# Performance work log

Hardware: AMD Instinct MI355X
Metric: run time of the kernel (lower is better)

Reference implementation:

```python
import jax, jax.numpy as jnp
from jax import lax
import numpy as np

# ---- init hyperparameters (from init_kwargs) ----
STRIDE = 1
DP_CHANNELS = 1
ATOM_R = 8
ATOM_C = 8
NUMB_ATOM = 128
T_SC = 3
K = 256
BATCH = 32
IMG = 64


def setup_inputs() -> dict:
    key = jax.random.key(0)
    k1, k2 = jax.random.split(key)
    Y = jax.random.normal(k1, (BATCH, DP_CHANNELS, IMG, IMG), dtype=jnp.float32)
    # ConvTranspose2d weight layout: (numb_atom, dp_channels, atom_c, atom_r)
    W = jax.random.normal(k2, (NUMB_ATOM, DP_CHANNELS, ATOM_C, ATOM_R), dtype=jnp.float32)
    # normalise_weights(): each (i, j) filter divided by its L2 norm
    W = W / jnp.sqrt(jnp.sum(W ** 2, axis=(2, 3), keepdims=True))
    return {"Y": Y, "W_D": W}


def _conv_D(X, W):
    # PyTorch ConvTranspose2d (stride=1, no padding): full convolution with
    # spatially-flipped kernel; W is (in=numb_atom, out=dp_channels, kh, kw).
    kh, kw = W.shape[2], W.shape[3]
    return lax.conv_general_dilated(
        X, jnp.flip(W, (2, 3)), (1, 1),
        [(kh - 1, kh - 1), (kw - 1, kw - 1)],
        dimension_numbers=('NCHW', 'IOHW', 'NCHW'))


def _conv_Dt(R, Wt):
    # PyTorch Conv2d (VALID, stride=1): Wt is (out=numb_atom, in=dp, kh, kw)
    return lax.conv_general_dilated(
        R, Wt, (1, 1), 'VALID', dimension_numbers=('NCHW', 'OIHW', 'NCHW'))


def _hard_threshold_k(X, k):
    # keep the k largest-|.| entries per sample (over flattened C,H,W)
    B = X.shape[0]
    flat = X.reshape(B, -1)
    _, idx = lax.top_k(jnp.abs(flat), k)                      # [B, k]
    vals = jnp.take_along_axis(flat, idx, axis=1)             # [B, k]
    out = jnp.zeros_like(flat).at[jnp.arange(B)[:, None], idx].set(vals)
    return out.reshape(X.shape)


def _linesearch(Y, X, W, Wt, k):
    R = Y - _conv_D(X, W)
    g = _conv_Dt(R, Wt)
    l2_start = jnp.sum(R ** 2)

    def attempt(alpha):
        Xu = _hard_threshold_k(X + alpha * g, k)
        err = jnp.sum((Y - _conv_D(Xu, W)) ** 2)
        return Xu, err

    Xu0, err0 = attempt(jnp.float32(1.0))

    def cond(s):
        _, _, err, count = s
        return (err >= l2_start) & (count <= 15)

    def body(s):
        alpha, _, _, count = s
        alpha = alpha * jnp.float32(0.5)
        Xu, err = attempt(alpha)
        return (alpha, Xu, err, count + 1)

    alpha, Xu, err, _ = lax.while_loop(
        cond, body, (jnp.float32(1.0), Xu0, err0, jnp.int32(0)))
    return Xu, err, alpha


def reference(Y, W_D):
    # D_trans.weight = D.weight.permute(0,1,3,2) -> (numb_atom, dp, atom_r, atom_c)
    Wt = jnp.swapaxes(W_D, 2, 3)
    kh, kw = Wt.shape[2], Wt.shape[3]
    B, _, H, W_sp = Y.shape
    X = jnp.zeros((B, W_D.shape[0], H - kh + 1, W_sp - kw + 1), dtype=Y.dtype)
    for _ in range(T_SC):
        X, _, _ = _linesearch(Y, X, W_D, Wt, K)
    return X
```

## Files before the change

### kernel.cpp

```cpp
#include <hip/hip_runtime.h>
#include <stdint.h>

#define NB   32
#define NCH  128
#define IMG  64
#define IMG2 4096
#define OH   57
#define OHW  3249
#define CHW  415872
#define KTOP 256
#define NATT 17
#define NS   32
#define SCAP 512
#define NCAP 1536
#define NBUCK 8192
#define HSHIFT 18
#define TGT  512
#define RSTRIDE 72
#define NZB  257
#define BMW  12996

typedef unsigned long long ull;

__global__ void k_init(int* support_cnt) {
    if (threadIdx.x < NB) support_cnt[threadIdx.x] = 0;
}

__global__ __launch_bounds__(256) void k_resid(
    const float* __restrict__ Y, const float* __restrict__ W,
    const int* __restrict__ support_cnt, const ull* __restrict__ sup_iv,
    float* __restrict__ Rg, double* __restrict__ l2part,
    uint32_t* __restrict__ hist, int* __restrict__ cand_cnt)
{
    int bx = blockIdx.x, tid = threadIdx.x;
    if (bx >= NB) {
        int zb = bx - NB;
        if (zb < 256) {
            ((uint4*)hist)[zb * 256 + tid] = make_uint4(0u, 0u, 0u, 0u);
        } else {
            ((uint4*)cand_cnt)[tid] = make_uint4(0u, 0u, 0u, 0u);
        }
        return;
    }
    int b = bx;
    __shared__ float Rs[IMG2];
    const float4* Y4 = (const float4*)(Y + b * IMG2);
    float4* R4 = (float4*)Rs;
    for (int i = tid; i < IMG2 / 4; i += 256) R4[i] = Y4[i];
    __syncthreads();
    int n = support_cnt[b];
    for (int task = tid; task < n * 64; task += 256) {
        int i = task >> 6, tap = task & 63, p = tap >> 3, q = tap & 7;
        ull iv = sup_iv[b * KTOP + i];
        uint32_t idx = (uint32_t)iv;
        float val = __uint_as_float((uint32_t)(iv >> 32));
        int c = idx / OHW, rem = idx % OHW, s = rem / OH, t = rem % OH;
        float w = W[c * 64 + p * 8 + q];
        atomicAdd(&Rs[(s + p) * IMG + (t + q)], -val * w);
    }
    __syncthreads();
    double acc = 0.0;
    for (int i = tid; i < IMG2; i += 256) {
        float v = Rs[i];
        Rg[b * IMG2 + i] = v;
        acc += (double)v * (double)v;
    }
    __shared__ double red[256];
    red[tid] = acc; __syncthreads();
    for (int s2 = 128; s2 > 0; s2 >>= 1) { if (tid < s2) red[tid] += red[tid + s2]; __syncthreads(); }
    if (tid == 0) l2part[b] = red[0];
}

__global__ __launch_bounds__(256) void k_conv(
    const float* __restrict__ Rg, const float* __restrict__ W,
    float* __restrict__ g_out, uint32_t* __restrict__ hist)
{
    int b = blockIdx.x, cg0 = blockIdx.y, tid = threadIdx.x;
    __shared__ float Rs[71 * 72];
    __shared__ uint32_t hl[NBUCK];
    for (int i = tid; i < 71 * 72; i += 256) Rs[i] = 0.f;
    for (int i = tid; i < NBUCK; i += 256) hl[i] = 0u;
    __syncthreads();
    const float4* R4 = (const float4*)(Rg + b * IMG2);
    for (int i = tid; i < 1024; i += 256) {
        int row = i >> 4, col4 = (i & 15) * 4;
        *(float4*)&Rs[row * 72 + col4] = R4[i];
    }
    __syncthreads();
    int csub = tid >> 7;
    int tile = tid & 127;
    bool active = tile < 120;
    int tr = active ? tile / 15 : 0;
    int tc = active ? tile % 15 : 0;
    int s0 = tr * 8, t0 = tc * 4;

    for (int sub = 0; sub < 4; ++sub) {
        int c = cg0 * 8 + sub * 2 + csub;
        int c_s = __builtin_amdgcn_readfirstlane(c);
        const float* Wc = W + c_s * 64;

        float acc[8][4];
#pragma unroll
        for (int r = 0; r < 8; ++r)
#pragma unroll
            for (int cc = 0; cc < 4; ++cc) acc[r][cc] = 0.f;

#pragma unroll
        for (int rho = 0; rho < 15; ++rho) {
            float rb[12];
            const float* rp = &Rs[(s0 + rho) * 72 + t0];
            *(float4*)&rb[0] = *(const float4*)rp;
            *(float4*)&rb[4] = *(const float4*)(rp + 4);
            *(float4*)&rb[8] = *(const float4*)(rp + 8);
#pragma unroll
            for (int r = 0; r < 8; ++r) {
                const int p = rho - r;
                if (p >= 0 && p < 8) {
#pragma unroll
                    for (int q = 0; q < 8; ++q) {
                        float wv = Wc[q * 8 + p];
#pragma unroll
                        for (int cc = 0; cc < 4; ++cc)
                            acc[r][cc] = fmaf(rb[cc + q], wv, acc[r][cc]);
                    }
                }
            }
        }
        if (active) {
            float* go = g_out + (size_t)(b * NCH + c) * OHW;
#pragma unroll
            for (int r = 0; r < 8; ++r) {
                int s = s0 + r;
                if (s < OH) {
#pragma unroll
                    for (int cc = 0; cc < 4; ++cc) {
                        int t = t0 + cc;
                        if (t < OH) {
                            float v = acc[r][cc];
                            go[s * OH + t] = v;
                            uint32_t bits = __float_as_uint(v) & 0x7fffffffu;
                            atomicAdd(&hl[bits >> HSHIFT], 1u);
                        }
                    }
                }
            }
        }
    }
    __syncthreads();
    for (int i = tid; i < NBUCK; i += 256) {
        uint32_t v = hl[i];
        if (v) atomicAdd(&hist[b * NBUCK + i], v);
    }
}

__global__ __launch_bounds__(256) void k_thresh(const uint32_t* __restrict__ hist,
                                                uint32_t* __restrict__ thr) {
    int b = blockIdx.x, tid = threadIdx.x;
    uint32_t h[32];
    uint32_t s = 0;
    const uint32_t* hb = hist + b * NBUCK + tid * 32;
#pragma unroll
    for (int k = 0; k < 32; ++k) { h[k] = hb[k]; s += h[k]; }
    __shared__ uint32_t buf[2][256];
    int cur = 0;
    buf[0][tid] = s;
    __syncthreads();
    for (int d = 1; d < 256; d <<= 1) {
        uint32_t v = buf[cur][tid];
        if (tid + d < 256) v += buf[cur][tid + d];
        buf[cur ^ 1][tid] = v;
        cur ^= 1;
        __syncthreads();
    }
    uint32_t sufme = buf[cur][tid];
    uint32_t base  = (tid < 255) ? buf[cur][tid + 1] : 0u;
    if (tid == 0 && buf[cur][0] < TGT) thr[b] = 0u;
    if (base < TGT && sufme >= TGT) {
        uint32_t acc = base; int bk = 0;
#pragma unroll
        for (int k = 31; k >= 0; --k) {
            acc += h[k];
            if (acc >= TGT) { bk = tid * 32 + k; break; }
        }
        thr[b] = (uint32_t)bk << HSHIFT;
    }
}

__global__ __launch_bounds__(256) void k_collect(
    const float* __restrict__ g, const uint32_t* __restrict__ thr,
    int* __restrict__ cand_cnt, uint32_t* __restrict__ cand_idx, float* __restrict__ cand_g)
{
    int b = blockIdx.y;
    int i4 = blockIdx.x * 256 + threadIdx.x;
    if (i4 >= CHW / 4) return;
    int slice = blockIdx.x & (NS - 1);
    uint32_t tb = thr[b];
    float4 v4 = ((const float4*)(g + (size_t)b * CHW))[i4];
    float vv[4] = { v4.x, v4.y, v4.z, v4.w };
#pragma unroll
    for (int k = 0; k < 4; ++k) {
        uint32_t bits = __float_as_uint(vv[k]) & 0x7fffffffu;
        if (bits >= tb) {
            int pos = atomicAdd(&cand_cnt[b * NS + slice], 1);
            if (pos < SCAP) {
                cand_idx[(b * NS + slice) * SCAP + pos] = (uint32_t)(i4 * 4 + k);
                cand_g[(b * NS + slice) * SCAP + pos] = vv[k];
            }
        }
    }
}

__global__ __launch_bounds__(1024) void k_suppg(
    const float* __restrict__ g,
    const int* __restrict__ support_cnt, const ull* __restrict__ sup_iv,
    const int* __restrict__ cand_cnt, const uint32_t* __restrict__ cand_idx,
    const float* __restrict__ cand_g,
    uint4* __restrict__ ns_pack, ull* __restrict__ sup_gp, ull* __restrict__ kb_all)
{
    int b = blockIdx.x, tid = threadIdx.x, lane = tid & 63;
    __shared__ uint32_t bm[BMW];
    __shared__ int cnts[NS];
    __shared__ ull ck[NCAP];
    __shared__ float cg_l[NCAP];
    __shared__ int nns_sh;
    int n = support_cnt[b];
    for (int i = tid; i < BMW / 4; i += 1024) ((uint4*)bm)[i] = make_uint4(0u, 0u, 0u, 0u);
    if (tid < NS) cnts[tid] = min(cand_cnt[b * NS + tid], SCAP);
    if (tid == 0) nns_sh = 0;
    __syncthreads();
    if (tid < KTOP) {
        float gv = 0.f, vs = 0.f;
        uint32_t nidx;
        if (tid < n) {
            ull iv = sup_iv[b * KTOP + tid];
            uint32_t idx = (uint32_t)iv;
            nidx = idx;
            vs = __uint_as_float((uint32_t)(iv >> 32));
            atomicOr(&bm[idx >> 5], 1u << (idx & 31));
            gv = g[(size_t)b * CHW + idx];
            int c = idx / OHW, r = idx % OHW, s = r / OH, t = r % OH;
            uint32_t pk = (uint32_t)((c << 12) | (s << 6) | t);
            sup_gp[b * KTOP + tid] = ((ull)__float_as_uint(gv) << 32) | (ull)pk;
        } else {
            nidx = (uint32_t)(CHW + tid);
            sup_gp[b * KTOP + tid] = 0ull;
        }
        ull klo = (ull)(uint32_t)(~nidx);
#pragma unroll
        for (int a2 = 0; a2 < NATT; ++a2) {
            float v2 = (tid < n) ? fmaf(ldexpf(1.f, -a2), gv, vs) : 0.f;
            kb_all[((size_t)a2 * NB + b) * KTOP + tid] =
                ((ull)(__float_as_uint(v2) & 0x7fffffffu) << 32) | klo;
        }
    }
    __syncthreads();
    for (int t0 = tid; t0 < NS * SCAP; t0 += 1024) {
        int s = t0 >> 9, j = t0 & (SCAP - 1);
        bool keep = false; uint32_t idx = 0; float gv = 0.f;
        if (j < cnts[s]) {
            idx = cand_idx[(b * NS + s) * SCAP + j];
            gv = cand_g[(b * NS + s) * SCAP + j];
            keep = ((bm[idx >> 5] >> (idx & 31)) & 1u) == 0u;
        }
        ull mk = __ballot(keep);
        if (mk) {
            int basep = 0;
            if (lane == 0) basep = atomicAdd(&nns_sh, (int)__popcll(mk));
            basep = __shfl(basep, 0, 64);
            if (keep) {
                int p = basep + (int)__popcll(mk & ((1ull << lane) - 1ull));
                if (p < NCAP) {
                    ck[p] = ((ull)(__float_as_uint(gv) & 0x7fffffffu) << 32) | (ull)(uint32_t)(~idx);
                    cg_l[p] = gv;
                }
            }
        }
    }
    __syncthreads();
    int nns = min(nns_sh, NCAP);
    int nns8 = (nns + 7) & ~7;
    for (int i = nns + tid; i < nns8; i += 1024) ck[i] = 0ull;
    __syncthreads();
    ull myk[2]; int myr[2];
#pragma unroll
    for (int q = 0; q < 2; ++q) { int i = tid + 1024 * q; myk[q] = (i < nns) ? ck[i] : 0ull; myr[q] = 0; }
    for (int j = 0; j < nns8; j += 8) {
        ull t0 = ck[j], t1 = ck[j+1], t2 = ck[j+2], t3 = ck[j+3];
        ull t4 = ck[j+4], t5 = ck[j+5], t6 = ck[j+6], t7 = ck[j+7];
#pragma unroll
        for (int q = 0; q < 2; ++q) {
            myr[q] += ((t0 > myk[q]) ? 1 : 0) + ((t1 > myk[q]) ? 1 : 0)
                    + ((t2 > myk[q]) ? 1 : 0) + ((t3 > myk[q]) ? 1 : 0)
                    + ((t4 > myk[q]) ? 1 : 0) + ((t5 > myk[q]) ? 1 : 0)
                    + ((t6 > myk[q]) ? 1 : 0) + ((t7 > myk[q]) ? 1 : 0);
        }
    }
#pragma unroll
    for (int q = 0; q < 2; ++q) {
        int i = tid + 1024 * q;
        if (i < nns && myr[q] < KTOP) {
            uint32_t idx = ~(uint32_t)myk[q];
            int r = myr[q];
            int c = idx / OHW, rr = idx % OHW, s = rr / OH, t = rr % OH;
            uint32_t pk = (uint32_t)((c << 12) | (s << 6) | t);
            ns_pack[b * KTOP + r] = make_uint4(idx, __float_as_uint(cg_l[i]), pk, 0u);
        }
    }
}

__global__ __launch_bounds__(512) void k_att2(
    const float* __restrict__ Y, const float* __restrict__ W,
    const int* __restrict__ support_cnt, const ull* __restrict__ sup_iv,
    const ull* __restrict__ sup_gp, const uint4* __restrict__ ns_pack,
    const ull* __restrict__ kb_all,
    uint32_t* __restrict__ sel_idx, float* __restrict__ sel_val, double* __restrict__ err)
{
    int a = blockIdx.x, b = blockIdx.y, tid = threadIdx.x;
    int lane = tid & 63, wid = tid >> 6;
    float alpha = ldexpf(1.f, -a);
    int n = support_cnt[b];

    __shared__ float recon[64 * RSTRIDE];
    __shared__ ull kA[KTOP];
    __shared__ ull s_pv[KTOP];
    __shared__ uint32_t s_idx[KTOP];
    __shared__ double redd[8];

    uint32_t myi = 0, mypk = 0;
    float myv = 0.f;
    ull myk = 0;
    if (tid < KTOP) {
        uint4 np = ns_pack[b * KTOP + tid];
        myi = np.x;
        myv = alpha * __uint_as_float(np.y);
        mypk = np.z;
        myk = ((ull)(__float_as_uint(myv) & 0x7fffffffu) << 32) | (ull)(uint32_t)(~myi);
        kA[tid] = myk;
    } else {
        int t2 = tid - KTOP;
        ull gp = sup_gp[b * KTOP + t2];
        ull iv = sup_iv[b * KTOP + t2];
        if (t2 < n) {
            myi = (uint32_t)iv;
            myv = fmaf(alpha, __uint_as_float((uint32_t)(gp >> 32)),
                       __uint_as_float((uint32_t)(iv >> 32)));
            mypk = (uint32_t)gp;
        } else {
            myi = (uint32_t)(CHW + t2);
            myv = 0.f; mypk = 0u;
        }
        myk = ((ull)(__float_as_uint(myv) & 0x7fffffffu) << 32) | (ull)(uint32_t)(~myi);
    }

    const float4* Y4 = (const float4*)(Y + b * IMG2);
    float4 y0 = Y4[tid * 2], y1 = Y4[tid * 2 + 1];

    for (int i = tid; i < 64 * RSTRIDE; i += 512) recon[i] = 0.f;
    __syncthreads();

    const ull* __restrict__ kb = kb_all + ((size_t)a * NB + b) * KTOP;
    int cb0 = 0, cb1 = 0;
    for (int j = 0; j < KTOP; j += 8) {
        ull t0 = kb[j],     t1 = kb[j + 1], t2 = kb[j + 2], t3 = kb[j + 3];
        ull t4 = kb[j + 4], t5 = kb[j + 5], t6 = kb[j + 6], t7 = kb[j + 7];
        cb0 += ((t0 > myk) ? 1 : 0) + ((t1 > myk) ? 1 : 0)
             + ((t2 > myk) ? 1 : 0) + ((t3 > myk) ? 1 : 0);
        cb1 += ((t4 > myk) ? 1 : 0) + ((t5 > myk) ? 1 : 0)
             + ((t6 > myk) ? 1 : 0) + ((t7 > myk) ? 1 : 0);
    }
    int cb = cb0 + cb1;
    int rank;
    if (tid < KTOP) {
        rank = tid + cb;
    } else {
        int lo = 0, hi = KTOP;
        while (lo < hi) { int mid = (lo + hi) >> 1; if (kA[mid] > myk) lo = mid + 1; else hi = mid; }
        rank = lo + cb;
    }
    if (rank < KTOP) {
        s_pv[rank] = ((ull)__float_as_uint(myv) << 32) | (ull)mypk;
        s_idx[rank] = myi;
    }
    __syncthreads();

    {
        int p = lane >> 3, q = lane & 7;
        ull pv[4]; float wv[4];
#pragma unroll
        for (int j = 0; j < 4; ++j) pv[j] = s_pv[wid + 8 * j];
#pragma unroll
        for (int j = 0; j < 4; ++j) wv[j] = W[(((uint32_t)pv[j]) >> 12) * 64 + lane];
#pragma unroll
        for (int k4 = 0; k4 < 32; k4 += 4) {
            ull npv[4] = {0, 0, 0, 0}; float nwv[4] = {0.f, 0.f, 0.f, 0.f};
            if (k4 + 4 < 32) {
#pragma unroll
                for (int j = 0; j < 4; ++j) npv[j] = s_pv[wid + 8 * (k4 + 4 + j)];
#pragma unroll
                for (int j = 0; j < 4; ++j) nwv[j] = W[(((uint32_t)npv[j]) >> 12) * 64 + lane];
            }
#pragma unroll
            for (int j = 0; j < 4; ++j) {
                uint32_t pk = (uint32_t)pv[j];
                float val = __uint_as_float((uint32_t)(pv[j] >> 32));
                int s = (pk >> 6) & 63, t = pk & 63;
                atomicAdd(&recon[(s + p) * RSTRIDE + (t + q)], val * wv[j]);
            }
#pragma unroll
            for (int j = 0; j < 4; ++j) { pv[j] = npv[j]; wv[j] = nwv[j]; }
        }
    }
    __syncthreads();

    double accd = 0.0;
    {
        int idx0 = tid * 2;
        const float* rr = &recon[(idx0 >> 4) * RSTRIDE + (idx0 & 15) * 4];
        float d0 = y0.x - rr[0]; accd += (double)d0 * (double)d0;
        float d1 = y0.y - rr[1]; accd += (double)d1 * (double)d1;
        float d2 = y0.z - rr[2]; accd += (double)d2 * (double)d2;
        float d3 = y0.w - rr[3]; accd += (double)d3 * (double)d3;
        int idx1 = tid * 2 + 1;
        rr = &recon[(idx1 >> 4) * RSTRIDE + (idx1 & 15) * 4];
        float e0 = y1.x - rr[0]; accd += (double)e0 * (double)e0;
        float e1 = y1.y - rr[1]; accd += (double)e1 * (double)e1;
        float e2 = y1.z - rr[2]; accd += (double)e2 * (double)e2;
        float e3 = y1.w - rr[3]; accd += (double)e3 * (double)e3;
    }
    for (int d = 32; d > 0; d >>= 1) accd += __shfl_xor(accd, d, 64);
    if (lane == 0) redd[wid] = accd;
    __syncthreads();
    if (tid == 0) {
        double e = 0.0;
#pragma unroll
        for (int w2 = 0; w2 < 8; ++w2) e += redd[w2];
        err[a * NB + b] = e;
    }

    if (tid < KTOP) {
        size_t o = ((size_t)a * NB + b) * KTOP;
        ull pvt = s_pv[tid];
        sel_idx[o + tid] = s_idx[tid];
        sel_val[o + tid] = __uint_as_float((uint32_t)(pvt >> 32));
    }
}

__global__ __launch_bounds__(256) void k_update(
    const double* __restrict__ l2part, const double* __restrict__ err,
    const uint32_t* __restrict__ sel_idx, const float* __restrict__ sel_val,
    int* __restrict__ support_cnt, ull* __restrict__ sup_iv)
{
    int b = blockIdx.x, tid = threadIdx.x;
    __shared__ double esum[NATT + 1];
    __shared__ int sel_sh;
    if (tid < NATT) {
        double e = 0.0;
        for (int b2 = 0; b2 < NB; ++b2) e += err[tid * NB + b2];
        esum[tid] = e;
    } else if (tid == NATT) {
        double l2 = 0.0;
        for (int b2 = 0; b2 < NB; ++b2) l2 += l2part[b2];
        esum[NATT] = l2;
    }
    __syncthreads();
    if (tid == 0) {
        double l2 = esum[NATT];
        int sel = NATT - 1;
        for (int a2 = 0; a2 < NATT; ++a2) if (esum[a2] < l2) { sel = a2; break; }
        sel_sh = sel;
    }
    __syncthreads();
    int a = sel_sh;
    __shared__ uint32_t ki[KTOP];
    __shared__ float kv[KTOP];
    ki[tid] = sel_idx[((size_t)a * NB + b) * KTOP + tid];
    kv[tid] = sel_val[((size_t)a * NB + b) * KTOP + tid];
    __syncthreads();
    uint32_t me = ki[tid];
    int rank = 0;
    for (int j = 0; j < KTOP; j += 8) {
        uint32_t a0 = ki[j], a1 = ki[j+1], a2 = ki[j+2], a3 = ki[j+3];
        uint32_t a4 = ki[j+4], a5 = ki[j+5], a6 = ki[j+6], a7 = ki[j+7];
        rank += ((a0 < me) ? 1 : 0) + ((a1 < me) ? 1 : 0) + ((a2 < me) ? 1 : 0) + ((a3 < me) ? 1 : 0)
              + ((a4 < me) ? 1 : 0) + ((a5 < me) ? 1 : 0) + ((a6 < me) ? 1 : 0) + ((a7 < me) ? 1 : 0);
    }
    sup_iv[b * KTOP + rank] = (ull)me | ((ull)__float_as_uint(kv[tid]) << 32);
    if (tid == 0) support_cnt[b] = KTOP;
}

__global__ void k_outzero(float4* __restrict__ out) {
    int i = blockIdx.x * 256 + threadIdx.x;
    if (i < (NB * CHW) / 4) out[i] = make_float4(0.f, 0.f, 0.f, 0.f);
}

__global__ void k_scatter(const ull* __restrict__ sup_iv, float* __restrict__ out) {
    int b = blockIdx.x, tid = threadIdx.x;
    if (tid < KTOP) {
        ull iv = sup_iv[b * KTOP + tid];
        out[(size_t)b * CHW + (uint32_t)iv] = __uint_as_float((uint32_t)(iv >> 32));
    }
}

static size_t align256(size_t x) { return (x + 255) & ~(size_t)255; }

extern "C" void kernel_launch(void* const* d_in, const int* in_sizes, int n_in,
                              void* d_out, int out_size, void* d_ws, size_t ws_size,
                              hipStream_t stream)
{
    const float* Y = (const float*)d_in[0];
    const float* W = (const float*)d_in[1];
    float* out = (float*)d_out;

    char* p = (char*)d_ws;
    size_t off = 0;
    auto carve = [&](size_t bytes) { void* r = p + off; off = align256(off + bytes); return r; };
    float*    Rg          = (float*)   carve(NB * IMG2 * sizeof(float));
    uint32_t* hist        = (uint32_t*)carve((size_t)NB * NBUCK * sizeof(uint32_t));
    uint32_t* thr         = (uint32_t*)carve(NB * sizeof(uint32_t));
    int*      cand_cnt    = (int*)     carve(NB * NS * sizeof(int));
    double*   l2part      = (double*)  carve(NB * sizeof(double));
    double*   err         = (double*)  carve(NATT * NB * sizeof(double));
    int*      support_cnt = (int*)     carve(NB * sizeof(int));
    ull*      sup_iv      = (ull*)     carve((size_t)NB * KTOP * sizeof(ull));
    uint32_t* sel_idx     = (uint32_t*)carve((size_t)NATT * NB * KTOP * sizeof(uint32_t));
    float*    sel_val     = (float*)   carve((size_t)NATT * NB * KTOP * sizeof(float));
    uint32_t* cand_idx    = (uint32_t*)carve((size_t)NB * NS * SCAP * sizeof(uint32_t));
    float*    cand_g      = (float*)   carve((size_t)NB * NS * SCAP * sizeof(float));
    uint4*    ns_pack     = (uint4*)   carve((size_t)NB * KTOP * sizeof(uint4));
    ull*      sup_gp      = (ull*)     carve((size_t)NB * KTOP * sizeof(ull));
    ull*      kb_all      = (ull*)     carve((size_t)NATT * NB * KTOP * sizeof(ull));
    (void)ws_size; (void)in_sizes; (void)n_in; (void)out_size;

    k_init<<<1, 64, 0, stream>>>(support_cnt);
    for (int t = 0; t < 3; ++t) {
        k_resid<<<NB + NZB, 256, 0, stream>>>(Y, W, support_cnt, sup_iv,
                                              Rg, l2part, hist, cand_cnt);
        k_conv<<<dim3(NB, 16), 256, 0, stream>>>(Rg, W, out, hist);
        k_thresh<<<NB, 256, 0, stream>>>(hist, thr);
        k_collect<<<dim3((CHW / 4 + 255) / 256, NB), 256, 0, stream>>>(out, thr, cand_cnt, cand_idx, cand_g);
        k_suppg<<<NB, 1024, 0, stream>>>(out, support_cnt, sup_iv,
                                         cand_cnt, cand_idx, cand_g,
                                         ns_pack, sup_gp, kb_all);
        k_att2<<<dim3(NATT, NB), 512, 0, stream>>>(Y, W, support_cnt, sup_iv,
                                                   sup_gp, ns_pack, kb_all,
                                                   sel_idx, sel_val, err);
        k_update<<<NB, 256, 0, stream>>>(l2part, err, sel_idx, sel_val,
                                         support_cnt, sup_iv);
    }
    k_outzero<<<((NB * CHW) / 4 + 255) / 256, 256, 0, stream>>>((float4*)out);
    k_scatter<<<NB, 256, 0, stream>>>(sup_iv, out);
}
```

Before: 662.4 us.

## Split attempt kernel into selection and reconstruction kernels

Splits the fused per-attempt kernel into k_sel and k_rec. k_sel uses 256 threads, each ranking one new candidate and one support entry against the kb table. k_rec loads the selected entries from global memory and does the reconstruction and error reduction. This should lighten register and shared-memory pressure and shorten the serial rank phase inside the heavy kernel. In exchange it adds a launch per iteration and a global round trip through new att_pv and att_idx buffers. The two sentinel index assignments for padded support slots conflict: the else branch sets CHW+tid+KTOP, then a following line overwrites it with CHW+tid. Since it is only a padding sentinel with zero value it likely does not matter.

```diff
diff --git a/kernel.cpp b/kernel.cpp
--- a/kernel.cpp
+++ b/kernel.cpp
@@ -308,79 +308,95 @@
     }
 }
 
-__global__ __launch_bounds__(512) void k_att2(
-    const float* __restrict__ Y, const float* __restrict__ W,
+__global__ __launch_bounds__(256) void k_sel(
     const int* __restrict__ support_cnt, const ull* __restrict__ sup_iv,
     const ull* __restrict__ sup_gp, const uint4* __restrict__ ns_pack,
     const ull* __restrict__ kb_all,
-    uint32_t* __restrict__ sel_idx, float* __restrict__ sel_val, double* __restrict__ err)
+    ull* __restrict__ att_pv, uint32_t* __restrict__ att_idx)
 {
     int a = blockIdx.x, b = blockIdx.y, tid = threadIdx.x;
-    int lane = tid & 63, wid = tid >> 6;
     float alpha = ldexpf(1.f, -a);
     int n = support_cnt[b];
 
-    __shared__ float recon[64 * RSTRIDE];
     __shared__ ull kA[KTOP];
-    __shared__ ull s_pv[KTOP];
-    __shared__ uint32_t s_idx[KTOP];
-    __shared__ double redd[8];
-
-    uint32_t myi = 0, mypk = 0;
-    float myv = 0.f;
-    ull myk = 0;
-    if (tid < KTOP) {
-        uint4 np = ns_pack[b * KTOP + tid];
-        myi = np.x;
-        myv = alpha * __uint_as_float(np.y);
-        mypk = np.z;
-        myk = ((ull)(__float_as_uint(myv) & 0x7fffffffu) << 32) | (ull)(uint32_t)(~myi);
-        kA[tid] = myk;
+
+    uint4 np = ns_pack[b * KTOP + tid];
+    uint32_t ni = np.x;
+    float nv = alpha * __uint_as_float(np.y);
+    uint32_t npk = np.z;
+    ull nk = ((ull)(__float_as_uint(nv) & 0x7fffffffu) << 32) | (ull)(uint32_t)(~ni);
+    kA[tid] = nk;
+
+    ull gp = sup_gp[b * KTOP + tid];
+    ull iv = sup_iv[b * KTOP + tid];
+    uint32_t si; float sv; uint32_t spk;
+    if (tid < n) {
+        si = (uint32_t)iv;
+        sv = fmaf(alpha, __uint_as_float((uint32_t)(gp >> 32)),
+                  __uint_as_float((uint32_t)(iv >> 32)));
+        spk = (uint32_t)gp;
     } else {
-        int t2 = tid - KTOP;
-        ull gp = sup_gp[b * KTOP + t2];
-        ull iv = sup_iv[b * KTOP + t2];
-        if (t2 < n) {
-            myi = (uint32_t)iv;
-            myv = fmaf(alpha, __uint_as_float((uint32_t)(gp >> 32)),
-                       __uint_as_float((uint32_t)(iv >> 32)));
-            mypk = (uint32_t)gp;
-        } else {
-            myi = (uint32_t)(CHW + t2);
-            myv = 0.f; mypk = 0u;
-        }
-        myk = ((ull)(__float_as_uint(myv) & 0x7fffffffu) << 32) | (ull)(uint32_t)(~myi);
-    }
-
-    const float4* Y4 = (const float4*)(Y + b * IMG2);
-    float4 y0 = Y4[tid * 2], y1 = Y4[tid * 2 + 1];
-
-    for (int i = tid; i < 64 * RSTRIDE; i += 512) recon[i] = 0.f;
+        si = (uint32_t)(CHW + tid + KTOP);
+        sv = 0.f; spk = 0u;
+    }
+    if (tid >= n) si = (uint32_t)(CHW + tid);
+    ull sk = ((ull)(__float_as_uint(sv) & 0x7fffffffu) << 32) | (ull)(uint32_t)(~si);
     __syncthreads();
 
     const ull* __restrict__ kb = kb_all + ((size_t)a * NB + b) * KTOP;
-    int cb0 = 0, cb1 = 0;
+    int cbn = 0, cbs = 0;
     for (int j = 0; j < KTOP; j += 8) {
         ull t0 = kb[j],     t1 = kb[j + 1], t2 = kb[j + 2], t3 = kb[j + 3];
         ull t4 = kb[j + 4], t5 = kb[j + 5], t6 = kb[j + 6], t7 = kb[j + 7];
-        cb0 += ((t0 > myk) ? 1 : 0) + ((t1 > myk) ? 1 : 0)
-             + ((t2 > myk) ? 1 : 0) + ((t3 > myk) ? 1 : 0);
-        cb1 += ((t4 > myk) ? 1 : 0) + ((t5 > myk) ? 1 : 0)
-             + ((t6 > myk) ? 1 : 0) + ((t7 > myk) ? 1 : 0);
-    }
-    int cb = cb0 + cb1;
-    int rank;
+        cbn += ((t0 > nk) ? 1 : 0) + ((t1 > nk) ? 1 : 0)
+             + ((t2 > nk) ? 1 : 0) + ((t3 > nk) ? 1 : 0)
+             + ((t4 > nk) ? 1 : 0) + ((t5 > nk) ? 1 : 0)
+             + ((t6 > nk) ? 1 : 0) + ((t7 > nk) ? 1 : 0);
+        cbs += ((t0 > sk) ? 1 : 0) + ((t1 > sk) ? 1 : 0)
+             + ((t2 > sk) ? 1 : 0) + ((t3 > sk) ? 1 : 0)
+             + ((t4 > sk) ? 1 : 0) + ((t5 > sk) ? 1 : 0)
+             + ((t6 > sk) ? 1 : 0) + ((t7 > sk) ? 1 : 0);
+    }
+    int rank_n = tid + cbn;
+    int lo = 0, hi = KTOP;
+    while (lo < hi) { int mid = (lo + hi) >> 1; if (kA[mid] > sk) lo = mid + 1; else hi = mid; }
+    int rank_s = lo + cbs;
+
+    size_t o = ((size_t)a * NB + b) * KTOP;
+    if (rank_n < KTOP) {
+        att_pv[o + rank_n] = ((ull)__float_as_uint(nv) << 32) | (ull)npk;
+        att_idx[o + rank_n] = ni;
+    }
+    if (rank_s < KTOP) {
+        att_pv[o + rank_s] = ((ull)__float_as_uint(sv) << 32) | (ull)spk;
+        att_idx[o + rank_s] = si;
+    }
+}
+
+__global__ __launch_bounds__(512) void k_rec(
+    const float* __restrict__ Y, const float* __restrict__ W,
+    const ull* __restrict__ att_pv, const uint32_t* __restrict__ att_idx,
+    uint32_t* __restrict__ sel_idx, float* __restrict__ sel_val, double* __restrict__ err)
+{
+    int a = blockIdx.x, b = blockIdx.y, tid = threadIdx.x;
+    int lane = tid & 63, wid = tid >> 6;
+
+    __shared__ float recon[64 * RSTRIDE];
+    __shared__ ull s_pv[KTOP];
+    __shared__ double redd[8];
+
+    size_t o = ((size_t)a * NB + b) * KTOP;
     if (tid < KTOP) {
-        rank = tid + cb;
-    } else {
-        int lo = 0, hi = KTOP;
-        while (lo < hi) { int mid = (lo + hi) >> 1; if (kA[mid] > myk) lo = mid + 1; else hi = mid; }
-        rank = lo + cb;
-    }
-    if (rank < KTOP) {
-        s_pv[rank] = ((ull)__float_as_uint(myv) << 32) | (ull)mypk;
-        s_idx[rank] = myi;
-    }
+        ull pv = att_pv[o + tid];
+        s_pv[tid] = pv;
+        sel_idx[o + tid] = att_idx[o + tid];
+        sel_val[o + tid] = __uint_as_float((uint32_t)(pv >> 32));
+    }
+
+    const float4* Y4 = (const float4*)(Y + b * IMG2);
+    float4 y0 = Y4[tid * 2], y1 = Y4[tid * 2 + 1];
+
+    for (int i = tid; i < 64 * RSTRIDE; i += 512) recon[i] = 0.f;
     __syncthreads();
 
     {
@@ -435,13 +451,6 @@
 #pragma unroll
         for (int w2 = 0; w2 < 8; ++w2) e += redd[w2];
         err[a * NB + b] = e;
-    }
-
-    if (tid < KTOP) {
-        size_t o = ((size_t)a * NB + b) * KTOP;
-        ull pvt = s_pv[tid];
-        sel_idx[o + tid] = s_idx[tid];
-        sel_val[o + tid] = __uint_as_float((uint32_t)(pvt >> 32));
     }
 }
 
@@ -529,6 +538,8 @@
     uint4*    ns_pack     = (uint4*)   carve((size_t)NB * KTOP * sizeof(uint4));
     ull*      sup_gp      = (ull*)     carve((size_t)NB * KTOP * sizeof(ull));
     ull*      kb_all      = (ull*)     carve((size_t)NATT * NB * KTOP * sizeof(ull));
+    ull*      att_pv      = (ull*)     carve((size_t)NATT * NB * KTOP * sizeof(ull));
+    uint32_t* att_idx     = (uint32_t*)carve((size_t)NATT * NB * KTOP * sizeof(uint32_t));
     (void)ws_size; (void)in_sizes; (void)n_in; (void)out_size;
 
     k_init<<<1, 64, 0, stream>>>(support_cnt);
@@ -541,9 +552,10 @@
         k_suppg<<<NB, 1024, 0, stream>>>(out, support_cnt, sup_iv,
                                          cand_cnt, cand_idx, cand_g,
                                          ns_pack, sup_gp, kb_all);
-        k_att2<<<dim3(NATT, NB), 512, 0, stream>>>(Y, W, support_cnt, sup_iv,
-                                                   sup_gp, ns_pack, kb_all,
-                                                   sel_idx, sel_val, err);
+        k_sel<<<dim3(NATT, NB), 256, 0, stream>>>(support_cnt, sup_iv, sup_gp,
+                                                  ns_pack, kb_all, att_pv, att_idx);
+        k_rec<<<dim3(NATT, NB), 512, 0, stream>>>(Y, W, att_pv, att_idx,
+                                                  sel_idx, sel_val, err);
         k_update<<<NB, 256, 0, stream>>>(l2part, err, sel_idx, sel_val,
                                          support_cnt, sup_iv);
     }
```

Measured after the change: 678.9 us. 2.5% more time.

## Fuse line-search attempts and update into cooperative kernel with early exit

Applied to the files above, without the earlier changes.

Replaces the kernel that evaluated all 17 step-size attempts in parallel, and the separate update kernel, with one cooperative kernel. It evaluates attempts in rounds of 8 per batch sample. After each round a grid-wide sync lets block 0 pick the first accepted step, and later rounds are skipped once one passes. The winning block writes the new support directly, which removes the intermediate selection buffers and one launch per iteration. In exchange it adds grid syncs, caps parallelism at 256 blocks, and writes the support in magnitude-rank order instead of index-sorted order.

```diff
diff --git a/kernel.cpp b/kernel.cpp
--- a/kernel.cpp
+++ b/kernel.cpp
@@ -1,5 +1,8 @@
 #include <hip/hip_runtime.h>
+#include <hip/hip_cooperative_groups.h>
 #include <stdint.h>
+
+namespace cg = cooperative_groups;
 
 #define NB   32
 #define NCH  128
@@ -10,6 +13,8 @@
 #define CHW  415872
 #define KTOP 256
 #define NATT 17
+#define NBATCH 8
+#define NROUNDS 3
 #define NS   32
 #define SCAP 512
 #define NCAP 1536
@@ -308,16 +313,16 @@
     }
 }
 
-__global__ __launch_bounds__(512) void k_att2(
+__global__ __launch_bounds__(512) void k_attc(
     const float* __restrict__ Y, const float* __restrict__ W,
-    const int* __restrict__ support_cnt, const ull* __restrict__ sup_iv,
+    int* __restrict__ support_cnt, ull* __restrict__ sup_iv,
     const ull* __restrict__ sup_gp, const uint4* __restrict__ ns_pack,
-    const ull* __restrict__ kb_all,
-    uint32_t* __restrict__ sel_idx, float* __restrict__ sel_val, double* __restrict__ err)
+    const ull* __restrict__ kb_all, const double* __restrict__ l2part,
+    double* __restrict__ err, int* __restrict__ ctrl)
 {
-    int a = blockIdx.x, b = blockIdx.y, tid = threadIdx.x;
-    int lane = tid & 63, wid = tid >> 6;
-    float alpha = ldexpf(1.f, -a);
+    cg::grid_group grid = cg::this_grid();
+    int tid = threadIdx.x, lane = tid & 63, wid = tid >> 6;
+    int b = blockIdx.x & (NB - 1), ar = blockIdx.x >> 5;
     int n = support_cnt[b];
 
     __shared__ float recon[64 * RSTRIDE];
@@ -325,167 +330,169 @@
     __shared__ ull s_pv[KTOP];
     __shared__ uint32_t s_idx[KTOP];
     __shared__ double redd[8];
-
-    uint32_t myi = 0, mypk = 0;
-    float myv = 0.f;
-    ull myk = 0;
-    if (tid < KTOP) {
-        uint4 np = ns_pack[b * KTOP + tid];
-        myi = np.x;
-        myv = alpha * __uint_as_float(np.y);
-        mypk = np.z;
-        myk = ((ull)(__float_as_uint(myv) & 0x7fffffffu) << 32) | (ull)(uint32_t)(~myi);
-        kA[tid] = myk;
-    } else {
-        int t2 = tid - KTOP;
-        ull gp = sup_gp[b * KTOP + t2];
-        ull iv = sup_iv[b * KTOP + t2];
-        if (t2 < n) {
-            myi = (uint32_t)iv;
-            myv = fmaf(alpha, __uint_as_float((uint32_t)(gp >> 32)),
-                       __uint_as_float((uint32_t)(iv >> 32)));
-            mypk = (uint32_t)gp;
-        } else {
-            myi = (uint32_t)(CHW + t2);
-            myv = 0.f; mypk = 0u;
-        }
-        myk = ((ull)(__float_as_uint(myv) & 0x7fffffffu) << 32) | (ull)(uint32_t)(~myi);
-    }
-
-    const float4* Y4 = (const float4*)(Y + b * IMG2);
-    float4 y0 = Y4[tid * 2], y1 = Y4[tid * 2 + 1];
-
-    for (int i = tid; i < 64 * RSTRIDE; i += 512) recon[i] = 0.f;
-    __syncthreads();
-
-    const ull* __restrict__ kb = kb_all + ((size_t)a * NB + b) * KTOP;
-    int cb0 = 0, cb1 = 0;
-    for (int j = 0; j < KTOP; j += 8) {
-        ull t0 = kb[j],     t1 = kb[j + 1], t2 = kb[j + 2], t3 = kb[j + 3];
-        ull t4 = kb[j + 4], t5 = kb[j + 5], t6 = kb[j + 6], t7 = kb[j + 7];
-        cb0 += ((t0 > myk) ? 1 : 0) + ((t1 > myk) ? 1 : 0)
-             + ((t2 > myk) ? 1 : 0) + ((t3 > myk) ? 1 : 0);
-        cb1 += ((t4 > myk) ? 1 : 0) + ((t5 > myk) ? 1 : 0)
-             + ((t6 > myk) ? 1 : 0) + ((t7 > myk) ? 1 : 0);
-    }
-    int cb = cb0 + cb1;
-    int rank;
-    if (tid < KTOP) {
-        rank = tid + cb;
-    } else {
-        int lo = 0, hi = KTOP;
-        while (lo < hi) { int mid = (lo + hi) >> 1; if (kA[mid] > myk) lo = mid + 1; else hi = mid; }
-        rank = lo + cb;
-    }
-    if (rank < KTOP) {
-        s_pv[rank] = ((ull)__float_as_uint(myv) << 32) | (ull)mypk;
-        s_idx[rank] = myi;
-    }
-    __syncthreads();
-
-    {
-        int p = lane >> 3, q = lane & 7;
-        ull pv[4]; float wv[4];
-#pragma unroll
-        for (int j = 0; j < 4; ++j) pv[j] = s_pv[wid + 8 * j];
-#pragma unroll
-        for (int j = 0; j < 4; ++j) wv[j] = W[(((uint32_t)pv[j]) >> 12) * 64 + lane];
-#pragma unroll
-        for (int k4 = 0; k4 < 32; k4 += 4) {
-            ull npv[4] = {0, 0, 0, 0}; float nwv[4] = {0.f, 0.f, 0.f, 0.f};
-            if (k4 + 4 < 32) {
-#pragma unroll
-                for (int j = 0; j < 4; ++j) npv[j] = s_pv[wid + 8 * (k4 + 4 + j)];
-#pragma unroll
-                for (int j = 0; j < 4; ++j) nwv[j] = W[(((uint32_t)npv[j]) >> 12) * 64 + lane];
-            }
-#pragma unroll
-            for (int j = 0; j < 4; ++j) {
-                uint32_t pk = (uint32_t)pv[j];
-                float val = __uint_as_float((uint32_t)(pv[j] >> 32));
-                int s = (pk >> 6) & 63, t = pk & 63;
-                atomicAdd(&recon[(s + p) * RSTRIDE + (t + q)], val * wv[j]);
-            }
-#pragma unroll
-            for (int j = 0; j < 4; ++j) { pv[j] = npv[j]; wv[j] = nwv[j]; }
-        }
-    }
-    __syncthreads();
-
-    double accd = 0.0;
-    {
-        int idx0 = tid * 2;
-        const float* rr = &recon[(idx0 >> 4) * RSTRIDE + (idx0 & 15) * 4];
-        float d0 = y0.x - rr[0]; accd += (double)d0 * (double)d0;
-        float d1 = y0.y - rr[1]; accd += (double)d1 * (double)d1;
-        float d2 = y0.z - rr[2]; accd += (double)d2 * (double)d2;
-        float d3 = y0.w - rr[3]; accd += (double)d3 * (double)d3;
-        int idx1 = tid * 2 + 1;
-        rr = &recon[(idx1 >> 4) * RSTRIDE + (idx1 & 15) * 4];
-        float e0 = y1.x - rr[0]; accd += (double)e0 * (double)e0;
-        float e1 = y1.y - rr[1]; accd += (double)e1 * (double)e1;
-        float e2 = y1.z - rr[2]; accd += (double)e2 * (double)e2;
-        float e3 = y1.w - rr[3]; accd += (double)e3 * (double)e3;
-    }
-    for (int d = 32; d > 0; d >>= 1) accd += __shfl_xor(accd, d, 64);
-    if (lane == 0) redd[wid] = accd;
-    __syncthreads();
-    if (tid == 0) {
-        double e = 0.0;
-#pragma unroll
-        for (int w2 = 0; w2 < 8; ++w2) e += redd[w2];
-        err[a * NB + b] = e;
-    }
-
-    if (tid < KTOP) {
-        size_t o = ((size_t)a * NB + b) * KTOP;
-        ull pvt = s_pv[tid];
-        sel_idx[o + tid] = s_idx[tid];
-        sel_val[o + tid] = __uint_as_float((uint32_t)(pvt >> 32));
-    }
-}
-
-__global__ __launch_bounds__(256) void k_update(
-    const double* __restrict__ l2part, const double* __restrict__ err,
-    const uint32_t* __restrict__ sel_idx, const float* __restrict__ sel_val,
-    int* __restrict__ support_cnt, ull* __restrict__ sup_iv)
-{
-    int b = blockIdx.x, tid = threadIdx.x;
-    __shared__ double esum[NATT + 1];
-    __shared__ int sel_sh;
-    if (tid < NATT) {
-        double e = 0.0;
-        for (int b2 = 0; b2 < NB; ++b2) e += err[tid * NB + b2];
-        esum[tid] = e;
-    } else if (tid == NATT) {
-        double l2 = 0.0;
-        for (int b2 = 0; b2 < NB; ++b2) l2 += l2part[b2];
-        esum[NATT] = l2;
-    }
-    __syncthreads();
-    if (tid == 0) {
-        double l2 = esum[NATT];
-        int sel = NATT - 1;
-        for (int a2 = 0; a2 < NATT; ++a2) if (esum[a2] < l2) { sel = a2; break; }
-        sel_sh = sel;
-    }
-    __syncthreads();
-    int a = sel_sh;
-    __shared__ uint32_t ki[KTOP];
-    __shared__ float kv[KTOP];
-    ki[tid] = sel_idx[((size_t)a * NB + b) * KTOP + tid];
-    kv[tid] = sel_val[((size_t)a * NB + b) * KTOP + tid];
-    __syncthreads();
-    uint32_t me = ki[tid];
-    int rank = 0;
-    for (int j = 0; j < KTOP; j += 8) {
-        uint32_t a0 = ki[j], a1 = ki[j+1], a2 = ki[j+2], a3 = ki[j+3];
-        uint32_t a4 = ki[j+4], a5 = ki[j+5], a6 = ki[j+6], a7 = ki[j+7];
-        rank += ((a0 < me) ? 1 : 0) + ((a1 < me) ? 1 : 0) + ((a2 < me) ? 1 : 0) + ((a3 < me) ? 1 : 0)
-              + ((a4 < me) ? 1 : 0) + ((a5 < me) ? 1 : 0) + ((a6 < me) ? 1 : 0) + ((a7 < me) ? 1 : 0);
-    }
-    sup_iv[b * KTOP + rank] = (ull)me | ((ull)__float_as_uint(kv[tid]) << 32);
-    if (tid == 0) support_cnt[b] = KTOP;
+    __shared__ double esum_sh[NATT + 1];
+
+    int my_a = -1;
+    int a_sel = NATT - 1;
+
+    for (int round = 0; round < NROUNDS; ++round) {
+        int a = round * NBATCH + ar;
+        if (a < NATT) {
+            my_a = a;
+            float alpha = ldexpf(1.f, -a);
+            uint32_t myi = 0, mypk = 0;
+            float myv = 0.f;
+            ull myk = 0;
+            if (tid < KTOP) {
+                uint4 np = ns_pack[b * KTOP + tid];
+                myi = np.x;
+                myv = alpha * __uint_as_float(np.y);
+                mypk = np.z;
+                myk = ((ull)(__float_as_uint(myv) & 0x7fffffffu) << 32) | (ull)(uint32_t)(~myi);
+                kA[tid] = myk;
+            } else {
+                int t2 = tid - KTOP;
+                ull gp = sup_gp[b * KTOP + t2];
+                ull iv = sup_iv[b * KTOP + t2];
+                if (t2 < n) {
+                    myi = (uint32_t)iv;
+                    myv = fmaf(alpha, __uint_as_float((uint32_t)(gp >> 32)),
+                               __uint_as_float((uint32_t)(iv >> 32)));
+                    mypk = (uint32_t)gp;
+                } else {
+                    myi = (uint32_t)(CHW + t2);
+                    myv = 0.f; mypk = 0u;
+                }
+                myk = ((ull)(__float_as_uint(myv) & 0x7fffffffu) << 32) | (ull)(uint32_t)(~myi);
+            }
+            const float4* Y4 = (const float4*)(Y + b * IMG2);
+            float4 y0 = Y4[tid * 2], y1 = Y4[tid * 2 + 1];
+            for (int i = tid; i < 64 * RSTRIDE; i += 512) recon[i] = 0.f;
+            __syncthreads();
+
+            const ull* __restrict__ kb = kb_all + ((size_t)a * NB + b) * KTOP;
+            int cb0 = 0, cb1 = 0;
+            for (int j = 0; j < KTOP; j += 8) {
+                ull t0 = kb[j],     t1 = kb[j + 1], t2 = kb[j + 2], t3 = kb[j + 3];
+                ull t4 = kb[j + 4], t5 = kb[j + 5], t6 = kb[j + 6], t7 = kb[j + 7];
+                cb0 += ((t0 > myk) ? 1 : 0) + ((t1 > myk) ? 1 : 0)
+                     + ((t2 > myk) ? 1 : 0) + ((t3 > myk) ? 1 : 0);
+                cb1 += ((t4 > myk) ? 1 : 0) + ((t5 > myk) ? 1 : 0)
+                     + ((t6 > myk) ? 1 : 0) + ((t7 > myk) ? 1 : 0);
+            }
+            int cb = cb0 + cb1;
+            int rank;
+            if (tid < KTOP) {
+                rank = tid + cb;
+            } else {
+                int lo = 0, hi = KTOP;
+                while (lo < hi) { int mid = (lo + hi) >> 1; if (kA[mid] > myk) lo = mid + 1; else hi = mid; }
+                rank = lo + cb;
+            }
+            if (rank < KTOP) {
+                s_pv[rank] = ((ull)__float_as_uint(myv) << 32) | (ull)mypk;
+                s_idx[rank] = myi;
+            }
+            __syncthreads();
+
+            {
+                int p = lane >> 3, q = lane & 7;
+                ull pv[4]; float wv[4];
+#pragma unroll
+                for (int j = 0; j < 4; ++j) pv[j] = s_pv[wid + 8 * j];
+#pragma unroll
+                for (int j = 0; j < 4; ++j) wv[j] = W[(((uint32_t)pv[j]) >> 12) * 64 + lane];
+#pragma unroll
+                for (int k4 = 0; k4 < 32; k4 += 4) {
+                    ull npv[4] = {0, 0, 0, 0}; float nwv[4] = {0.f, 0.f, 0.f, 0.f};
+                    if (k4 + 4 < 32) {
+#pragma unroll
+                        for (int j = 0; j < 4; ++j) npv[j] = s_pv[wid + 8 * (k4 + 4 + j)];
+#pragma unroll
+                        for (int j = 0; j < 4; ++j) nwv[j] = W[(((uint32_t)npv[j]) >> 12) * 64 + lane];
+                    }
+#pragma unroll
+                    for (int j = 0; j < 4; ++j) {
+                        uint32_t pk = (uint32_t)pv[j];
+                        float val = __uint_as_float((uint32_t)(pv[j] >> 32));
+                        int s = (pk >> 6) & 63, t = pk & 63;
+                        atomicAdd(&recon[(s + p) * RSTRIDE + (t + q)], val * wv[j]);
+                    }
+#pragma unroll
+                    for (int j = 0; j < 4; ++j) { pv[j] = npv[j]; wv[j] = nwv[j]; }
+                }
+            }
+            __syncthreads();
+
+            double accd = 0.0;
+            {
+                int idx0 = tid * 2;
+                const float* rr = &recon[(idx0 >> 4) * RSTRIDE + (idx0 & 15) * 4];
+                float d0 = y0.x - rr[0]; accd += (double)d0 * (double)d0;
+                float d1 = y0.y - rr[1]; accd += (double)d1 * (double)d1;
+                float d2 = y0.z - rr[2]; accd += (double)d2 * (double)d2;
+                float d3 = y0.w - rr[3]; accd += (double)d3 * (double)d3;
+                int idx1 = tid * 2 + 1;
+                rr = &recon[(idx1 >> 4) * RSTRIDE + (idx1 & 15) * 4];
+                float e0 = y1.x - rr[0]; accd += (double)e0 * (double)e0;
+                float e1 = y1.y - rr[1]; accd += (double)e1 * (double)e1;
+                float e2 = y1.z - rr[2]; accd += (double)e2 * (double)e2;
+                float e3 = y1.w - rr[3]; accd += (double)e3 * (double)e3;
+            }
+            for (int d = 32; d > 0; d >>= 1) accd += __shfl_xor(accd, d, 64);
+            if (lane == 0) redd[wid] = accd;
+            __syncthreads();
+            if (tid == 0) {
+                double e = 0.0;
+#pragma unroll
+                for (int w2 = 0; w2 < 8; ++w2) e += redd[w2];
+                err[a * NB + b] = e;
+            }
+        }
+        __threadfence();
+        grid.sync();
+
+        if (blockIdx.x == 0) {
+            int eval = min(NBATCH * (round + 1), NATT);
+            if (tid < NATT) {
+                double e = 0.0;
+                if (tid < eval) {
+#pragma unroll 8
+                    for (int b2 = 0; b2 < NB; ++b2) e += err[tid * NB + b2];
+                }
+                esum_sh[tid] = e;
+            } else if (tid == NATT) {
+                double l2 = 0.0;
+#pragma unroll 8
+                for (int b2 = 0; b2 < NB; ++b2) l2 += l2part[b2];
+                esum_sh[NATT] = l2;
+            }
+            __syncthreads();
+            if (tid == 0) {
+                double l2 = esum_sh[NATT];
+                int sel = -1;
+                for (int a2 = 0; a2 < eval; ++a2) if (esum_sh[a2] < l2) { sel = a2; break; }
+                int done = (sel >= 0 || eval >= NATT) ? 1 : 0;
+                if (sel < 0) sel = NATT - 1;
+                __hip_atomic_store(&ctrl[0], sel, __ATOMIC_RELEASE, __HIP_MEMORY_SCOPE_AGENT);
+                __hip_atomic_store(&ctrl[1], done, __ATOMIC_RELEASE, __HIP_MEMORY_SCOPE_AGENT);
+            }
+        }
+        __threadfence();
+        grid.sync();
+
+        int done = __hip_atomic_load(&ctrl[1], __ATOMIC_ACQUIRE, __HIP_MEMORY_SCOPE_AGENT);
+        a_sel = __hip_atomic_load(&ctrl[0], __ATOMIC_ACQUIRE, __HIP_MEMORY_SCOPE_AGENT);
+        if (done) break;
+    }
+
+    if (my_a == a_sel) {
+        if (tid < KTOP) {
+            ull pvt = s_pv[tid];
+            sup_iv[b * KTOP + tid] = ((pvt >> 32) << 32) | (ull)s_idx[tid];
+        }
+        if (tid == 0) support_cnt[b] = KTOP;
+    }
 }
 
 __global__ void k_outzero(float4* __restrict__ out) {
@@ -519,16 +526,15 @@
     uint32_t* thr         = (uint32_t*)carve(NB * sizeof(uint32_t));
     int*      cand_cnt    = (int*)     carve(NB * NS * sizeof(int));
     double*   l2part      = (double*)  carve(NB * sizeof(double));
-    double*   err         = (double*)  carve(NATT * NB * sizeof(double));
+    double*   err         = (double*)  carve((size_t)NATT * NB * sizeof(double));
     int*      support_cnt = (int*)     carve(NB * sizeof(int));
     ull*      sup_iv      = (ull*)     carve((size_t)NB * KTOP * sizeof(ull));
-    uint32_t* sel_idx     = (uint32_t*)carve((size_t)NATT * NB * KTOP * sizeof(uint32_t));
-    float*    sel_val     = (float*)   carve((size_t)NATT * NB * KTOP * sizeof(float));
     uint32_t* cand_idx    = (uint32_t*)carve((size_t)NB * NS * SCAP * sizeof(uint32_t));
     float*    cand_g      = (float*)   carve((size_t)NB * NS * SCAP * sizeof(float));
     uint4*    ns_pack     = (uint4*)   carve((size_t)NB * KTOP * sizeof(uint4));
     ull*      sup_gp      = (ull*)     carve((size_t)NB * KTOP * sizeof(ull));
     ull*      kb_all      = (ull*)     carve((size_t)NATT * NB * KTOP * sizeof(ull));
+    int*      ctrl        = (int*)     carve(2 * sizeof(int));
     (void)ws_size; (void)in_sizes; (void)n_in; (void)out_size;
 
     k_init<<<1, 64, 0, stream>>>(support_cnt);
@@ -541,11 +547,13 @@
         k_suppg<<<NB, 1024, 0, stream>>>(out, support_cnt, sup_iv,
                                          cand_cnt, cand_idx, cand_g,
                                          ns_pack, sup_gp, kb_all);
-        k_att2<<<dim3(NATT, NB), 512, 0, stream>>>(Y, W, support_cnt, sup_iv,
-                                                   sup_gp, ns_pack, kb_all,
-                                                   sel_idx, sel_val, err);
-        k_update<<<NB, 256, 0, stream>>>(l2part, err, sel_idx, sel_val,
-                                         support_cnt, sup_iv);
+        {
+            void* args[] = { (void*)&Y, (void*)&W, (void*)&support_cnt, (void*)&sup_iv,
+                             (void*)&sup_gp, (void*)&ns_pack, (void*)&kb_all,
+                             (void*)&l2part, (void*)&err, (void*)&ctrl };
+            hipLaunchCooperativeKernel((const void*)k_attc, dim3(NBATCH * NB), dim3(512),
+                                       args, 0, stream);
+        }
     }
     k_outzero<<<((NB * CHW) / 4 + 255) / 256, 256, 0, stream>>>((float4*)out);
     k_scatter<<<NB, 256, 0, stream>>>(sup_iv, out);
```

Result: slower. 1.733 ms (+161.7%).
